# Kernel optimization log

Measured on AMD Instinct MI355X. Metric: run time of the kernel, lower is better.

## Reference

```python
import jax, jax.numpy as jnp
import numpy as np

B, T, D, H = 32, 1024, 1024, 128


def setup_inputs() -> dict:
    key = jax.random.key(0)
    k = jax.random.split(key, 5)
    s = 1.0 / np.sqrt(H)  # pytorch LSTM init scale
    return {
        "x": jax.random.normal(k[0], (B, T, D), dtype=jnp.float32),
        "W_ih": jax.random.uniform(k[1], (4 * H, D), minval=-s, maxval=s, dtype=jnp.float32),
        "W_hh": jax.random.uniform(k[2], (4 * H, H), minval=-s, maxval=s, dtype=jnp.float32),
        "b_ih": jax.random.uniform(k[3], (4 * H,), minval=-s, maxval=s, dtype=jnp.float32),
        "b_hh": jax.random.uniform(k[4], (4 * H,), minval=-s, maxval=s, dtype=jnp.float32),
    }


def reference(x, W_ih, W_hh, b_ih, b_hh):
    # x: [B, T, D]. Single-layer unidirectional LSTM, batch_first, zero init state.
    # Gate order matches PyTorch: i, f, g, o.
    b, t, d = x.shape
    h = W_hh.shape[1]
    # Fuse the input-side GEMM across all timesteps: [B, T, 4H]
    gx = jnp.einsum('btd,gd->btg', x, W_ih) + b_ih + b_hh

    def step(carry, g_t):
        h_prev, c_prev = carry
        g = g_t + h_prev @ W_hh.T  # [B, 4H]
        i, f, gg, o = jnp.split(g, 4, axis=-1)
        i = jax.nn.sigmoid(i)
        f = jax.nn.sigmoid(f)
        gg = jnp.tanh(gg)
        o = jax.nn.sigmoid(o)
        c = f * c_prev + i * gg
        hn = o * jnp.tanh(c)
        return (hn, c), hn

    h0 = jnp.zeros((b, h), dtype=x.dtype)
    c0 = jnp.zeros((b, h), dtype=x.dtype)
    (h_n, c_n), hs = jax.lax.scan(step, (h0, c0), jnp.swapaxes(gx, 0, 1))
    out = jnp.swapaxes(hs, 0, 1)  # [B, T, H]
    # Mirrors torch: (output, (h_n[1,B,H], c_n[1,B,H]))
    return out, h_n[None], c_n[None]
```

## Files before the change

### kernel.cpp

```cpp
#include <hip/hip_runtime.h>
#include <hip/hip_fp16.h>
#include <cstdint>
#include <cstddef>


typedef __attribute__((ext_vector_type(8))) _Float16 half8;
typedef __attribute__((ext_vector_type(4))) _Float16 half4;
typedef __attribute__((ext_vector_type(4))) float    f32x4;

#define BT    32768
#define DD    1024
#define GG    512
#define HH    128
#define TT    1024
#define BB    32

__global__ void prep_kernel(const float* __restrict__ wih,
                            const float* __restrict__ whh,
                            const float* __restrict__ bih,
                            const float* __restrict__ bhh,
                            _Float16* __restrict__ wih_h,
                            __half*   __restrict__ whh_h,
                            float* __restrict__ bsum) {
    int i = blockIdx.x * 256 + threadIdx.x;
    wih_h[i] = (_Float16)wih[i];
    if (i < GG * HH) whh_h[i] = __float2half(whh[i]);
    if (i < GG)      bsum[i] = bih[i] + bhh[i];
}

#define BM 128
#define BN 128
#define BK 32
#define LDP 40

__global__ __launch_bounds__(256)
void gemm_gx(const float* __restrict__ x, const _Float16* __restrict__ wih_h,
             const float* __restrict__ bsum, float* __restrict__ gx) {
    const int bid = blockIdx.x;
    const int m0 = (bid >> 2) * BM;
    const int n0 = (bid & 3) * BN;
    const int t  = threadIdx.x;
    const int lane = t & 63;
    const int w  = t >> 6;
    const int wr = w >> 1, wc = w & 1;
    const int lr = lane & 15;
    const int lk = lane >> 4;

    __shared__ __align__(16) _Float16 As[BM][LDP];
    __shared__ __align__(16) _Float16 Bs[BN][LDP];

    f32x4 acc[4][4] = {};

    for (int kt = 0; kt < DD; kt += BK) {
        #pragma unroll
        for (int pass = 0; pass < 4; ++pass) {
            int r = pass * 32 + (t >> 3);
            int c = (t & 7) * 4;
            float4 v = *(const float4*)(x + (size_t)(m0 + r) * DD + kt + c);
            half4 hv;
            hv[0] = (_Float16)v.x; hv[1] = (_Float16)v.y;
            hv[2] = (_Float16)v.z; hv[3] = (_Float16)v.w;
            *(half4*)&As[r][c] = hv;
        }
        #pragma unroll
        for (int pass = 0; pass < 2; ++pass) {
            int r = pass * 64 + (t >> 2);
            int c = (t & 3) * 8;
            float4 v = *(const float4*)(wih_h + (size_t)(n0 + r) * DD + kt + c);
            *(float4*)&Bs[r][c] = v;
        }
        __syncthreads();

        half8 af[4], bf[4];
        #pragma unroll
        for (int i = 0; i < 4; ++i)
            af[i] = *(const half8*)&As[wr * 64 + i * 16 + lr][lk * 8];
        #pragma unroll
        for (int j = 0; j < 4; ++j)
            bf[j] = *(const half8*)&Bs[wc * 64 + j * 16 + lr][lk * 8];

        #pragma unroll
        for (int i = 0; i < 4; ++i)
            #pragma unroll
            for (int j = 0; j < 4; ++j)
                acc[i][j] = __builtin_amdgcn_mfma_f32_16x16x32_f16(af[i], bf[j], acc[i][j], 0, 0, 0);
        __syncthreads();
    }

    #pragma unroll
    for (int j = 0; j < 4; ++j) {
        int n = n0 + wc * 64 + j * 16 + lr;
        float bn = bsum[n];
        #pragma unroll
        for (int i = 0; i < 4; ++i) {
            int mbase = m0 + wr * 64 + i * 16 + lk * 4;
            #pragma unroll
            for (int r = 0; r < 4; ++r)
                gx[(size_t)(mbase + r) * GG + n] = acc[i][j][r] + bn;
        }
    }
}

union F4H { float4 f; __half2 h[4]; };

__global__ __launch_bounds__(512)
void lstm_rec(const float* __restrict__ gx, const __half* __restrict__ whh_h,
              float* __restrict__ out, float* __restrict__ hn, float* __restrict__ cn) {
    const int b  = blockIdx.x;
    const int t  = threadIdx.x;
    const int j  = t >> 2;
    const int gi = t & 3;
    const int r  = gi * HH + j;

    __shared__ __align__(16) __half hbuf[2][HH];

    __half2 wv[64];
    {
        const float4* wp = (const float4*)(whh_h + (size_t)r * HH);
        #pragma unroll
        for (int q = 0; q < 16; ++q) {
            F4H u; u.f = wp[q];
            wv[4 * q + 0] = u.h[0]; wv[4 * q + 1] = u.h[1];
            wv[4 * q + 2] = u.h[2]; wv[4 * q + 3] = u.h[3];
        }
    }

    const float kneg = (gi == 2) ? -2.f : -1.f;
    const float k2   = (gi == 2) ?  2.f :  1.f;
    const float k3   = (gi == 2) ? -1.f :  0.f;

    if (t < HH) hbuf[0][t] = __float2half(0.f);
    __syncthreads();

    const float* gxp  = gx + (size_t)b * TT * GG + r;
    float*       outp = out + (size_t)b * TT * HH;

    float c = 0.f, hval = 0.f;
    float pre_cur = gxp[0];

    for (int step = 0; step < TT; ++step) {
        int sp = step + 1; if (sp >= TT) sp = TT - 1;
        float pre_nxt = gxp[(size_t)sp * GG];

        const float4* hp = (const float4*)hbuf[step & 1];
        __half2 acc[8];
        #pragma unroll
        for (int k = 0; k < 8; ++k) acc[k] = __float2half2_rn(0.f);
        #pragma unroll
        for (int q = 0; q < 16; ++q) {
            F4H u; u.f = hp[q];
            const int ab = (q & 1) * 4;
            acc[ab + 0] = __hfma2(wv[4 * q + 0], u.h[0], acc[ab + 0]);
            acc[ab + 1] = __hfma2(wv[4 * q + 1], u.h[1], acc[ab + 1]);
            acc[ab + 2] = __hfma2(wv[4 * q + 2], u.h[2], acc[ab + 2]);
            acc[ab + 3] = __hfma2(wv[4 * q + 3], u.h[3], acc[ab + 3]);
        }
        acc[0] = __hadd2(acc[0], acc[4]); acc[1] = __hadd2(acc[1], acc[5]);
        acc[2] = __hadd2(acc[2], acc[6]); acc[3] = __hadd2(acc[3], acc[7]);
        acc[0] = __hadd2(acc[0], acc[2]); acc[1] = __hadd2(acc[1], acc[3]);
        acc[0] = __hadd2(acc[0], acc[1]);
        float pre = pre_cur + __low2float(acc[0]) + __high2float(acc[0]);

        float s = __builtin_amdgcn_rcpf(1.f + __expf(pre * kneg));
        float a = fmaf(k2, s, k3);

        float x1 = __shfl_xor(a, 1);
        float x2 = __shfl_xor(a, 2);
        float x3 = __shfl_xor(x1, 2);

        if (gi == 0) {
            c = fmaf(x1, c, a * x2);
            float th = fmaf(2.f, __builtin_amdgcn_rcpf(1.f + __expf(-2.f * c)), -1.f);
            hval = x3 * th;
            hbuf[(step + 1) & 1][j] = __float2half(hval);
            outp[(size_t)step * HH + j] = hval;
        }

        __builtin_amdgcn_sched_barrier(0);
        asm volatile("s_waitcnt lgkmcnt(0)" ::: "memory");
        __builtin_amdgcn_s_barrier();
        __builtin_amdgcn_sched_barrier(0);

        pre_cur = pre_nxt;
    }

    if (gi == 0) {
        hn[b * HH + j] = hval;
        cn[b * HH + j] = c;
    }
}

extern "C" void kernel_launch(void* const* d_in, const int* in_sizes, int n_in,
                              void* d_out, int out_size, void* d_ws, size_t ws_size,
                              hipStream_t stream) {
    const float* x   = (const float*)d_in[0];
    const float* wih = (const float*)d_in[1];
    const float* whh = (const float*)d_in[2];
    const float* bih = (const float*)d_in[3];
    const float* bhh = (const float*)d_in[4];
    float* out = (float*)d_out;

    char* ws = (char*)d_ws;
    _Float16* wih_h = (_Float16*)ws;
    __half*   whh_h = (__half*)(ws + (size_t)(1 << 20));
    float*    bsum  = (float*)(ws + (size_t)(1 << 20) + (128 << 10));
    float*    gx    = (float*)(ws + (size_t)(1 << 20) + (128 << 10) + 4096);

    prep_kernel<<<(GG * DD) / 256, 256, 0, stream>>>(wih, whh, bih, bhh, wih_h, whh_h, bsum);
    gemm_gx<<<(BT / BM) * (GG / BN), 256, 0, stream>>>(x, wih_h, bsum, gx);

    float* hn = out + (size_t)BB * TT * HH;
    float* cn = hn + BB * HH;
    lstm_rec<<<BB, 512, 0, stream>>>(gx, whh_h, out, hn, cn);
}
```

Baseline: 749.0 us.

## Stage LSTM outputs in shared ring, swap shuffles for DPP, deepen gx prefetch

```diff
diff --git a/kernel.cpp b/kernel.cpp
--- a/kernel.cpp
+++ b/kernel.cpp
@@ -101,9 +101,21 @@
     }
 }
 
-union F4H { float4 f; __half2 h[4]; };
-
-__global__ __launch_bounds__(512)
+
+__device__ __forceinline__ __half2 u2h(uint32_t v) { return *(__half2*)&v; }
+
+template <int CTRL>
+__device__ __forceinline__ float dpp_qp(float x) {
+    int i = __float_as_int(x);
+    i = __builtin_amdgcn_update_dpp(0, i, CTRL, 0xF, 0xF, true);
+    return __int_as_float(i);
+}
+#define QP_XOR1 0xB1
+#define QP_XOR2 0x4E
+
+#define LOG2E   1.4426950408889634f
+
+__global__ __launch_bounds__(512, 1)
 void lstm_rec(const float* __restrict__ gx, const __half* __restrict__ whh_h,
               float* __restrict__ out, float* __restrict__ hn, float* __restrict__ cn) {
     const int b  = blockIdx.x;
@@ -113,21 +125,24 @@
     const int r  = gi * HH + j;
 
     __shared__ __align__(16) __half hbuf[2][HH];
-
-    __half2 wv[64];
+    __shared__ __align__(16) float  oring[64][HH];
+
+    uint32_t wv[64];
     {
-        const float4* wp = (const float4*)(whh_h + (size_t)r * HH);
+        const uint4* wp = (const uint4*)(whh_h + (size_t)r * HH);
         #pragma unroll
         for (int q = 0; q < 16; ++q) {
-            F4H u; u.f = wp[q];
-            wv[4 * q + 0] = u.h[0]; wv[4 * q + 1] = u.h[1];
-            wv[4 * q + 2] = u.h[2]; wv[4 * q + 3] = u.h[3];
-        }
-    }
-
-    const float kneg = (gi == 2) ? -2.f : -1.f;
-    const float k2   = (gi == 2) ?  2.f :  1.f;
-    const float k3   = (gi == 2) ? -1.f :  0.f;
+            uint4 u = wp[q];
+            wv[4 * q + 0] = u.x; wv[4 * q + 1] = u.y;
+            wv[4 * q + 2] = u.z; wv[4 * q + 3] = u.w;
+        }
+    }
+    #pragma unroll
+    for (int q = 0; q < 64; ++q) asm volatile("" : "+v"(wv[q]));
+
+    const float kneg = (gi == 2) ? -2.f * LOG2E : -LOG2E;
+    const float k2   = (gi == 2) ?  2.f : 1.f;
+    const float k3   = (gi == 2) ? -1.f : 0.f;
 
     if (t < HH) hbuf[0][t] = __float2half(0.f);
     __syncthreads();
@@ -136,44 +151,45 @@
     float*       outp = out + (size_t)b * TT * HH;
 
     float c = 0.f, hval = 0.f;
-    float pre_cur = gxp[0];
+    float p0 = gxp[0];
+    float p1 = gxp[GG];
 
     for (int step = 0; step < TT; ++step) {
-        int sp = step + 1; if (sp >= TT) sp = TT - 1;
-        float pre_nxt = gxp[(size_t)sp * GG];
-
-        const float4* hp = (const float4*)hbuf[step & 1];
+        int sp = step + 2; if (sp > TT - 1) sp = TT - 1;
+        float p2 = gxp[(size_t)sp * GG];
+
+        const uint4* hp = (const uint4*)hbuf[step & 1];
         __half2 acc[8];
         #pragma unroll
         for (int k = 0; k < 8; ++k) acc[k] = __float2half2_rn(0.f);
         #pragma unroll
         for (int q = 0; q < 16; ++q) {
-            F4H u; u.f = hp[q];
+            uint4 hv4 = hp[q];
             const int ab = (q & 1) * 4;
-            acc[ab + 0] = __hfma2(wv[4 * q + 0], u.h[0], acc[ab + 0]);
-            acc[ab + 1] = __hfma2(wv[4 * q + 1], u.h[1], acc[ab + 1]);
-            acc[ab + 2] = __hfma2(wv[4 * q + 2], u.h[2], acc[ab + 2]);
-            acc[ab + 3] = __hfma2(wv[4 * q + 3], u.h[3], acc[ab + 3]);
+            acc[ab + 0] = __hfma2(u2h(wv[4 * q + 0]), u2h(hv4.x), acc[ab + 0]);
+            acc[ab + 1] = __hfma2(u2h(wv[4 * q + 1]), u2h(hv4.y), acc[ab + 1]);
+            acc[ab + 2] = __hfma2(u2h(wv[4 * q + 2]), u2h(hv4.z), acc[ab + 2]);
+            acc[ab + 3] = __hfma2(u2h(wv[4 * q + 3]), u2h(hv4.w), acc[ab + 3]);
         }
         acc[0] = __hadd2(acc[0], acc[4]); acc[1] = __hadd2(acc[1], acc[5]);
         acc[2] = __hadd2(acc[2], acc[6]); acc[3] = __hadd2(acc[3], acc[7]);
         acc[0] = __hadd2(acc[0], acc[2]); acc[1] = __hadd2(acc[1], acc[3]);
         acc[0] = __hadd2(acc[0], acc[1]);
-        float pre = pre_cur + __low2float(acc[0]) + __high2float(acc[0]);
-
-        float s = __builtin_amdgcn_rcpf(1.f + __expf(pre * kneg));
+        float pre = p0 + __low2float(acc[0]) + __high2float(acc[0]);
+
+        float s = __builtin_amdgcn_rcpf(1.f + exp2f(pre * kneg));
         float a = fmaf(k2, s, k3);
 
-        float x1 = __shfl_xor(a, 1);
-        float x2 = __shfl_xor(a, 2);
-        float x3 = __shfl_xor(x1, 2);
+        float x1 = dpp_qp<QP_XOR1>(a);
+        float x2 = dpp_qp<QP_XOR2>(a);
+        float x3 = dpp_qp<QP_XOR2>(x1);
 
         if (gi == 0) {
             c = fmaf(x1, c, a * x2);
-            float th = fmaf(2.f, __builtin_amdgcn_rcpf(1.f + __expf(-2.f * c)), -1.f);
+            float th = fmaf(2.f, __builtin_amdgcn_rcpf(1.f + exp2f(-2.f * LOG2E * c)), -1.f);
             hval = x3 * th;
             hbuf[(step + 1) & 1][j] = __float2half(hval);
-            outp[(size_t)step * HH + j] = hval;
+            oring[step & 63][j] = hval;
         }
 
         __builtin_amdgcn_sched_barrier(0);
@@ -181,7 +197,16 @@
         __builtin_amdgcn_s_barrier();
         __builtin_amdgcn_sched_barrier(0);
 
-        pre_cur = pre_nxt;
+        if ((step & 63) == 63) {
+            float4*       dst = (float4*)(outp + (size_t)(step - 63) * HH);
+            const float4* src = (const float4*)&oring[0][0];
+            #pragma unroll
+            for (int k = 0; k < 4; ++k)
+                dst[t + k * 512] = src[t + k * 512];
+            __syncthreads();
+        }
+
+        p0 = p1; p1 = p2;
     }
 
     if (gi == 0) {
```

Result: slower. 843.5 us (+12.6%).
